# Performance work log

Hardware: AMD Instinct MI355X
Metric: run time of the kernel (lower is better)

Reference implementation:

```python
import jax, jax.numpy as jnp
import numpy as np

H = 16
W = 16
THRESH = 1.0
B = 32

# NOTE: [5.0, 1.0] reproduces the (likely buggy) constant in the original source.
SRC_POINTS = jnp.array([[0.0,0.0],[0.5,0.0],[1.0,0.0],[0.0,0.5],[0.5,0.5],[1.0,0.5],[0.0,1.0],[5.0,1.0],[1.0,1.0]], dtype=jnp.float32)

def _conv(x, w, stride, padding):
    return jax.lax.conv_general_dilated(x, w, (stride, stride), padding, dimension_numbers=('NHWC', 'HWIO', 'NHWC'))

def _tps_u(r):
    return r * r * jnp.log(r + 1e-6)

def _pdist(a, b):
    # a [...,2], b [n,2] -> [..., n] euclidean distances (eps for sqrt-at-0 safety)
    return jnp.sqrt(jnp.sum((a[..., None, :] - b) ** 2, axis=-1) + 1e-12)

def _tps_fit(ctrl, values):
    # cheind/py-thin-plate-spline TPS.fit with reduced=True. ctrl [n,2], values [n] -> theta [n+2]
    n = ctrl.shape[0]
    K = _tps_u(_pdist(ctrl, ctrl))
    P = jnp.concatenate([jnp.ones((n, 1), ctrl.dtype), ctrl], axis=1)
    A = jnp.zeros((n + 3, n + 3), ctrl.dtype)
    A = A.at[:n, :n].set(K).at[:n, n:].set(P).at[n:, :n].set(P.T)
    v = jnp.zeros(n + 3, ctrl.dtype).at[:n].set(values)
    theta = jnp.linalg.solve(A, v)
    return theta[1:]

def _tps_z(pts, ctrl, theta):
    # pts [m,2], theta reduced [n+2] -> [m]
    U = _tps_u(_pdist(pts, ctrl))
    w, a = theta[:-3], theta[-3:]
    w = jnp.concatenate([-jnp.sum(w, keepdims=True), w])
    return U @ w + a[0] + pts[:, 0] * a[1] + pts[:, 1] * a[2]

def _inlier_mask(geo):
    # geo [18] -> mask [H, W, H, W], mask[a_y, a_x, b_y, b_x]
    mv = geo.reshape(9, 2)
    dst = SRC_POINTS + mv
    delta = SRC_POINTS - dst  # c_src - c_dst (tps_theta_from_points)
    th_x = _tps_fit(dst, delta[:, 0])
    th_y = _tps_fit(dst, delta[:, 1])
    xs = jnp.linspace(0.0, 1.0, W)
    ys = jnp.linspace(0.0, 1.0, H)
    gx, gy = jnp.meshgrid(xs, ys)  # [H, W], gx varies along b_x
    pts = jnp.stack([gx.ravel(), gy.ravel()], axis=-1)
    ax = (gx + _tps_z(pts, dst, th_x).reshape(H, W)) * (H - 1)  # grid[...,0]*(map_size[0]-1)
    ay = (gy + _tps_z(pts, dst, th_y).reshape(H, W)) * (W - 1)
    # integer x in [ceil(ax-t), floor(ax+t)] clipped to [0,W-1]  <=>  |x - ax| <= t for x in range
    ix = jnp.arange(W, dtype=ax.dtype)
    iy = jnp.arange(H, dtype=ay.dtype)
    mx = jnp.abs(ix[:, None, None] - ax[None]) <= THRESH  # [W(a_x), H(b_y), W(b_x)]
    my = jnp.abs(iy[:, None, None] - ay[None]) <= THRESH  # [H(a_y), H(b_y), W(b_x)]
    return (my[:, None] & mx[None]).astype(jnp.float32)   # [H, W, H, W]

def _forward(image_A, image_B, W1, W2, W3, W4, Wr1, Wr2, Wd, bd):
    def feat(img):
        x = jax.nn.relu(_conv(img, W1, 2, 'SAME'))   # 256 -> 128
        x = jax.nn.relu(_conv(x, W2, 2, 'SAME'))     # 128 -> 64
        x = jax.nn.relu(_conv(x, W3, 2, 'SAME'))     # 64 -> 32
        x = jax.nn.relu(_conv(x, W4, 2, 'SAME'))     # 32 -> 16
        return x / (jnp.linalg.norm(x, axis=-1, keepdims=True) + 1e-6)  # channelwise l2 norm
    fA = feat(image_A)
    fB = feat(image_B)
    corr = jnp.einsum('bijc,bklc->bijkl', fA, fB)    # [B, H, W, H, W]
    b = corr.shape[0]
    r = corr.reshape(b, H, W, H * W)
    r = jax.nn.relu(_conv(r, Wr1, 1, 'VALID'))       # 16 -> 10
    r = jax.nn.relu(_conv(r, Wr2, 1, 'VALID'))       # 10 -> 6
    geo = r.reshape(b, -1) @ Wd + bd                 # [B, 18]
    # tf.numpy_function blocks gradients -> stop_gradient on the mask path
    masks = jax.lax.stop_gradient(jax.vmap(_inlier_mask)(geo))
    return jnp.sum(corr * masks, axis=(1, 2, 3, 4))  # [B]

def setup_inputs():
    key = jax.random.key(0)
    ks = jax.random.split(key, 10)
    s = 0.05
    return {
        'image_A': jax.random.normal(ks[0], (B, 256, 256, 3), jnp.float32),
        'image_B': jax.random.normal(ks[1], (B, 256, 256, 3), jnp.float32),
        'W1': jax.random.normal(ks[2], (3, 3, 3, 64), jnp.float32) * s,
        'W2': jax.random.normal(ks[3], (3, 3, 64, 128), jnp.float32) * s,
        'W3': jax.random.normal(ks[4], (3, 3, 128, 256), jnp.float32) * s,
        'W4': jax.random.normal(ks[5], (3, 3, 256, 512), jnp.float32) * s,
        'Wr1': jax.random.normal(ks[6], (7, 7, 256, 128), jnp.float32) * s,
        'Wr2': jax.random.normal(ks[7], (5, 5, 128, 64), jnp.float32) * s,
        'Wd': jax.random.normal(ks[8], (2304, 18), jnp.float32) * s,
        'bd': jnp.zeros((18,), jnp.float32),
    }

def reference(image_A, image_B, W1, W2, W3, W4, Wr1, Wr2, Wd, bd):
    return _forward(image_A, image_B, W1, W2, W3, W4, Wr1, Wr2, Wd, bd)
```

## Files before the change

kernel.cpp:

```cpp
#include <hip/hip_runtime.h>
#include <math.h>


typedef __attribute__((ext_vector_type(8))) _Float16 f16x8;
typedef __attribute__((ext_vector_type(4))) _Float16 f16x4;
typedef __attribute__((ext_vector_type(4))) float f32x4;

__device__ __forceinline__ unsigned short f2h(float f) {
  return __builtin_bit_cast(unsigned short, (_Float16)f);
}

__device__ __forceinline__ void gl16(const unsigned short* g, _Float16* l) {
  auto* gp = (const __attribute__((address_space(1))) unsigned int*)(g);
  auto* lp = (__attribute__((address_space(3))) unsigned int*)(l);
  __builtin_amdgcn_global_load_lds(gp, lp, 16, 0, 0);
}

__global__ __launch_bounds__(256) void prep_all(
    const float* __restrict__ W1, const float* __restrict__ W2,
    const float* __restrict__ W3, const float* __restrict__ W4,
    const float* __restrict__ Wr1, const float* __restrict__ Wr2,
    unsigned short* __restrict__ WT1, unsigned short* __restrict__ WT2,
    unsigned short* __restrict__ WT3, unsigned short* __restrict__ WT4,
    unsigned short* __restrict__ WTr1, unsigned short* __restrict__ WTr2,
    float* __restrict__ ZPf) {
  long idx = (long)blockIdx.x * 256 + threadIdx.x;
  if (idx < 1024) { ZPf[idx] = 0.f; return; }
  idx -= 1024;
  if (idx < 2048) {
    const int o = (int)idx >> 5, k = (int)idx & 31;
    WT1[idx] = (k < 27) ? f2h(W1[(size_t)k * 64 + o]) : (unsigned short)0;
    return;
  }
  idx -= 2048;
  if (idx < 73728) {
    const int k = (int)idx / 128, o = (int)idx % 128;
    WT2[(size_t)o * 576 + k] = f2h(W2[idx]);
    return;
  }
  idx -= 73728;
  if (idx < 294912) {
    const int k = (int)idx / 256, o = (int)idx % 256;
    WT3[(size_t)o * 1152 + k] = f2h(W3[idx]);
    return;
  }
  idx -= 294912;
  if (idx < 1179648) {
    const int k = (int)idx / 512, o = (int)idx % 512;
    WT4[(size_t)o * 2304 + k] = f2h(W4[idx]);
    return;
  }
  idx -= 1179648;
  if (idx < 1605632) {
    const int k = (int)idx / 128, o = (int)idx % 128;
    WTr1[(size_t)o * 12544 + k] = f2h(Wr1[idx]);
    return;
  }
  idx -= 1605632;
  if (idx < 204800) {
    const int k = (int)idx / 64, o = (int)idx % 64;
    WTr2[(size_t)o * 3200 + k] = f2h(Wr2[idx]);
  }
}

__global__ __launch_bounds__(256) void conv1_mfma(const float* __restrict__ inA,
                                                  const float* __restrict__ inB,
                                                  const unsigned short* __restrict__ wt1,
                                                  unsigned short* __restrict__ out) {
  const int i = blockIdx.x;
  const int b = blockIdx.y;
  const int tid = threadIdx.x;
  const int lane = tid & 63, wid = tid >> 6;
  const int lrow = lane & 15, quad = lane >> 4;

  __shared__ _Float16 Rows[3][776];
  __shared__ _Float16 OutB[8192];

  const float* __restrict__ img = (b < 32) ? inA : inB;
  const float* __restrict__ inb = img + (size_t)(b & 31) * 196608;
  const f16x4 z4 = {0, 0, 0, 0};
#pragma unroll
  for (int di = 0; di < 3; ++di) {
    const int y = 2 * i + di;
    if (tid < 192) {
      f16x4 h4 = z4;
      if (y < 256) {
        const float4 v4 = *(const float4*)(inb + (size_t)y * 768 + tid * 4);
        h4[0] = (_Float16)v4.x; h4[1] = (_Float16)v4.y;
        h4[2] = (_Float16)v4.z; h4[3] = (_Float16)v4.w;
      }
      *(f16x4*)&Rows[di][tid * 4] = h4;
    }
    if (tid < 3) Rows[di][768 + tid] = (_Float16)0.f;
  }
  __syncthreads();

  f16x8 bf[4];
#pragma unroll
  for (int ni = 0; ni < 4; ++ni)
    bf[ni] = *(const f16x8*)(wt1 + (ni * 16 + lrow) * 32 + quad * 8);

  f16x8 af[2];
#pragma unroll
  for (int mi = 0; mi < 2; ++mi) {
    const int j = wid * 32 + mi * 16 + lrow;
#pragma unroll
    for (int s = 0; s < 8; ++s) {
      const int k = quad * 8 + s;
      if (k < 27) {
        const int di = k / 9, dj = (k / 3) % 3, c = k % 3;
        af[mi][s] = Rows[di][(2 * j + dj) * 3 + c];
      } else {
        af[mi][s] = (_Float16)0.f;
      }
    }
  }

  f32x4 acc[2][4];
#pragma unroll
  for (int mi = 0; mi < 2; ++mi)
#pragma unroll
    for (int ni = 0; ni < 4; ++ni) {
      const f32x4 z = {0.f, 0.f, 0.f, 0.f};
      acc[mi][ni] = __builtin_amdgcn_mfma_f32_16x16x32_f16(af[mi], bf[ni], z, 0, 0, 0);
    }

#pragma unroll
  for (int mi = 0; mi < 2; ++mi)
#pragma unroll
    for (int ni = 0; ni < 4; ++ni)
#pragma unroll
      for (int r = 0; r < 4; ++r) {
        const int j = wid * 32 + mi * 16 + quad * 4 + r;
        const int ch = ni * 16 + lrow;
        OutB[j * 64 + (ch ^ (((j >> 2) & 3) << 4))] =
            (_Float16)fmaxf(acc[mi][ni][r], 0.f);
      }
  __syncthreads();

  unsigned short* __restrict__ ob = out + (((size_t)b * 128 + i) * 128) * 64;
#pragma unroll
  for (int q2 = 0; q2 < 4; ++q2) {
    const int v = tid + 256 * q2;
    const int j = v >> 3, c0 = (v & 7) * 8;
    const f16x8 pack = *(const f16x8*)&OutB[j * 64 + (c0 ^ (((j >> 2) & 3) << 4))];
    *(f16x8*)&ob[(size_t)j * 64 + c0] = pack;
  }
}

template <int BM, int BN, int CIN, int COUT, int KH, int KW, int STRIDE,
          int SAMEPAD, int SPLIT, int SK, int BATB, int OUTF32, int RELU>
__global__ __launch_bounds__(256) void tile_conv(
    const unsigned short* __restrict__ in, const unsigned short* __restrict__ wt,
    unsigned short* __restrict__ outh, float* __restrict__ outf,
    const unsigned short* __restrict__ zp,
    int Hin, int Win, int Hout, int Wout, int aLo, int bLo) {
  constexpr int CPT = CIN / 64;
  constexpr int LA = BM / 32;
  constexpr int LB = BN / 32;
  constexpr int KTOT = KH * KW * CIN;
  constexpr int MT = BM / 32;
  constexpr int NT = BN / 32;
  constexpr int PL = 1 + SPLIT;
  constexpr int LPS = PL * (LA + LB);
  constexpr unsigned WCN =
      (unsigned)((LPS & 0xF) | (0x7 << 4) | (0xF << 8) | ((LPS >> 4) << 14));
  constexpr unsigned WC0 = (unsigned)((0x7 << 4) | (0xF << 8));
  __shared__ _Float16 As[2][PL * BM * 64];
  __shared__ _Float16 Bs[2][PL * BN * 64];
  static_assert(SK > 1 || (size_t)BM * BN <= sizeof(As) / sizeof(_Float16),
                "bounce must fit in As");

  const int t = threadIdx.x;
  const int lane = t & 63, wid = t >> 6;
  const int lrow = lane & 15, quad = lane >> 4;
  const int m0 = blockIdx.x * BM;
  const int n0 = blockIdx.y * BN;

  const int q8 = ((t & 7) ^ ((t >> 3) & 7)) * 8;

  int pixB[LA], iS[LA], jS[LA];
#pragma unroll
  for (int i = 0; i < LA; ++i) {
    const int r = (t >> 3) + 32 * i;
    const int m = m0 + r;
    const int j = m % Wout;
    const int t2 = m / Wout;
    const int ii = t2 % Hout;
    const int b = t2 / Hout;
    iS[i] = ii * STRIDE;
    jS[i] = j * STRIDE;
    pixB[i] = ((b * Hin + iS[i]) * Win + jS[i]) * CIN + q8;
  }
  const unsigned short* wb = wt;
  if (BATB) wb += (size_t)(m0 / (Hout * Wout)) * COUT * KTOT;
  int bofB[LB];
#pragma unroll
  for (int i = 0; i < LB; ++i) {
    const int r = (t >> 3) + 32 * i;
    bofB[i] = (n0 + r) * KTOT + q8;
  }

  f32x4 acc[MT][NT];
#pragma unroll
  for (int mi = 0; mi < MT; ++mi)
#pragma unroll
    for (int ni = 0; ni < NT; ++ni) acc[mi][ni] = {0.f, 0.f, 0.f, 0.f};

  const int mB = (wid >> 1) * (BM / 2);
  const int nB = (wid & 1) * (BN / 2);

  int tap_lo = 0, tap_hi = KH * KW;
  if (SK > 1) {
    tap_lo = (int)blockIdx.z * KH * KW / SK;
    tap_hi = ((int)blockIdx.z + 1) * KH * KW / SK;
  }
  const int ch_lo = tap_lo * CPT, ch_hi = tap_hi * CPT;

  auto stage = [&](int buf, int ch) {
    const int tap = ch / CPT;
    const int c0 = (ch % CPT) * 64;
    const int di = tap / KW, dj = tap % KW;
    const int toff = (di * Win + dj) * CIN + c0;
    const int woff = tap * CIN + c0;
#pragma unroll
    for (int i = 0; i < LA; ++i) {
      const bool ok = !SAMEPAD || ((iS[i] + di < Hin) && (jS[i] + dj < Win));
      const unsigned short* s0 = ok ? in + pixB[i] + toff : zp + q8;
      gl16(s0, &As[buf][t * 8 + 2048 * i]);
      if (SPLIT) {
        const unsigned short* s1 = ok ? in + pixB[i] + toff + aLo : zp + q8;
        gl16(s1, &As[buf][BM * 64 + t * 8 + 2048 * i]);
      }
    }
#pragma unroll
    for (int i = 0; i < LB; ++i) {
      gl16(wb + bofB[i] + woff, &Bs[buf][t * 8 + 2048 * i]);
      if (SPLIT)
        gl16(wb + bofB[i] + woff + bLo, &Bs[buf][BN * 64 + t * 8 + 2048 * i]);
    }
  };

  stage(0, ch_lo);
  if (ch_lo + 1 < ch_hi) stage(1, ch_lo + 1);
  int cur = 0;
  for (int ch = ch_lo; ch < ch_hi; ++ch) {
    if (ch + 1 < ch_hi) __builtin_amdgcn_s_waitcnt(WCN);
    else __builtin_amdgcn_s_waitcnt(WC0);
    __builtin_amdgcn_sched_barrier(0);
    __builtin_amdgcn_s_barrier();
    __builtin_amdgcn_sched_barrier(0);
#pragma unroll
    for (int ks = 0; ks < 2; ++ks) {
      f16x8 af[MT], bf[NT], al[MT], bl[NT];
#pragma unroll
      for (int mi = 0; mi < MT; ++mi) {
        const int row = mB + mi * 16 + lrow;
        const int off = row * 64 + (((ks * 4 + quad) ^ (row & 7)) * 8);
        af[mi] = *(const f16x8*)&As[cur][off];
        if (SPLIT) al[mi] = *(const f16x8*)&As[cur][BM * 64 + off];
      }
#pragma unroll
      for (int ni = 0; ni < NT; ++ni) {
        const int row = nB + ni * 16 + lrow;
        const int off = row * 64 + (((ks * 4 + quad) ^ (row & 7)) * 8);
        bf[ni] = *(const f16x8*)&Bs[cur][off];
        if (SPLIT) bl[ni] = *(const f16x8*)&Bs[cur][BN * 64 + off];
      }
#pragma unroll
      for (int mi = 0; mi < MT; ++mi)
#pragma unroll
        for (int ni = 0; ni < NT; ++ni) {
          if (SPLIT) {
            acc[mi][ni] = __builtin_amdgcn_mfma_f32_16x16x32_f16(af[mi], bl[ni],
                                                                 acc[mi][ni], 0, 0, 0);
            acc[mi][ni] = __builtin_amdgcn_mfma_f32_16x16x32_f16(al[mi], bf[ni],
                                                                 acc[mi][ni], 0, 0, 0);
          }
          acc[mi][ni] = __builtin_amdgcn_mfma_f32_16x16x32_f16(af[mi], bf[ni],
                                                               acc[mi][ni], 0, 0, 0);
        }
    }
    __builtin_amdgcn_sched_barrier(0);
    __builtin_amdgcn_s_barrier();
    __builtin_amdgcn_sched_barrier(0);
    if (ch + 2 < ch_hi) stage(cur, ch + 2);
    cur ^= 1;
  }

  if (SK > 1) {
    const size_t slice = (size_t)blockIdx.z * ((size_t)gridDim.x * BM * COUT);
#pragma unroll
    for (int mi = 0; mi < MT; ++mi)
#pragma unroll
      for (int ni = 0; ni < NT; ++ni)
#pragma unroll
        for (int r = 0; r < 4; ++r) {
          const int row = m0 + mB + mi * 16 + quad * 4 + r;
          const int col = n0 + nB + ni * 16 + lrow;
          outf[slice + (size_t)row * COUT + col] = acc[mi][ni][r];
        }
  } else {
    _Float16* bounce = &As[0][0];
#pragma unroll
    for (int mi = 0; mi < MT; ++mi)
#pragma unroll
      for (int ni = 0; ni < NT; ++ni)
#pragma unroll
        for (int r = 0; r < 4; ++r) {
          const int row = mB + mi * 16 + quad * 4 + r;
          const int col = nB + ni * 16 + lrow;
          float v = acc[mi][ni][r];
          if (OUTF32) {
            outf[(size_t)(m0 + row) * COUT + n0 + col] = v;
          } else if (RELU) {
            v = fmaxf(v, 0.f);
          }
          bounce[row * BN + (col ^ (((row >> 2) & 3) << 4))] = (_Float16)v;
        }
    __syncthreads();
    constexpr int VPT = (BM * BN / 8) / 256;
#pragma unroll
    for (int q2 = 0; q2 < VPT; ++q2) {
      const int v = t + 256 * q2;
      const int rowL = v / (BN / 8);
      const int c0 = (v % (BN / 8)) * 8;
      const f16x8 pack =
          *(const f16x8*)&bounce[rowL * BN + (c0 ^ (((rowL >> 2) & 3) << 4))];
      *(f16x8*)&outh[(size_t)(m0 + rowL) * COUT + n0 + c0] = pack;
    }
  }
}

template <int MT, int NT, int CIN, int COUT, int KH, int KW, int SK>
__global__ __launch_bounds__(256) void gemm_conv(
    const unsigned short* __restrict__ in, const unsigned short* __restrict__ wt,
    float* __restrict__ outf, int Hin, int Win, int Hout, int Wout) {
  const int KTOT = KH * KW * CIN;
  const int lane = threadIdx.x & 63;
  const int wid = threadIdx.x >> 6;
  const int lrow = lane & 15;
  const int quad = lane >> 4;
  const int m0 = (blockIdx.x * 4 + wid) * (16 * MT);
  const int n0 = blockIdx.y * (16 * NT);

  int pix[MT];
#pragma unroll
  for (int mi = 0; mi < MT; ++mi) {
    const int m = m0 + mi * 16 + lrow;
    const int j = m % Wout;
    const int t = m / Wout;
    const int i = t % Hout;
    const int b = t / Hout;
    pix[mi] = (b * Hin + i) * Win + j;
  }
  const unsigned short* brow[NT];
#pragma unroll
  for (int ni = 0; ni < NT; ++ni)
    brow[ni] = wt + (size_t)(n0 + ni * 16 + lrow) * KTOT + quad * 8;

  f32x4 acc[MT][NT];
#pragma unroll
  for (int mi = 0; mi < MT; ++mi)
#pragma unroll
    for (int ni = 0; ni < NT; ++ni) acc[mi][ni] = {0.f, 0.f, 0.f, 0.f};

  const int tap_lo = (int)blockIdx.z * KH * KW / SK;
  const int tap_hi = ((int)blockIdx.z + 1) * KH * KW / SK;
  for (int tap = tap_lo; tap < tap_hi; ++tap) {
    const int di = tap / KW, dj = tap % KW;
    const unsigned short* ap[MT];
#pragma unroll
    for (int mi = 0; mi < MT; ++mi)
      ap[mi] = in + ((size_t)pix[mi] + di * Win + dj) * CIN + quad * 8;
    const int ko = tap * CIN;
#pragma unroll
    for (int c0 = 0; c0 < CIN; c0 += 32) {
      f16x8 ah[MT], bh[NT];
#pragma unroll
      for (int mi = 0; mi < MT; ++mi) ah[mi] = *(const f16x8*)(ap[mi] + c0);
#pragma unroll
      for (int ni = 0; ni < NT; ++ni) bh[ni] = *(const f16x8*)(brow[ni] + ko + c0);
#pragma unroll
      for (int mi = 0; mi < MT; ++mi)
#pragma unroll
        for (int ni = 0; ni < NT; ++ni)
          acc[mi][ni] = __builtin_amdgcn_mfma_f32_16x16x32_f16(ah[mi], bh[ni],
                                                               acc[mi][ni], 0, 0, 0);
    }
  }
  const size_t slice = (size_t)blockIdx.z * ((size_t)gridDim.x * 64 * MT * COUT);
#pragma unroll
  for (int mi = 0; mi < MT; ++mi)
#pragma unroll
    for (int ni = 0; ni < NT; ++ni)
#pragma unroll
      for (int r = 0; r < 4; ++r) {
        const int row = m0 + mi * 16 + quad * 4 + r;
        const int col = n0 + ni * 16 + lrow;
        outf[slice + (size_t)row * COUT + col] = acc[mi][ni][r];
      }
}

__global__ __launch_bounds__(256) void sum_relu_s(const float* __restrict__ p,
                                                  unsigned short* __restrict__ o,
                                                  int n, int parts) {
  const int idx = blockIdx.x * 256 + threadIdx.x;
  if (idx < n) {
    float v = 0.f;
    for (int s = 0; s < parts; ++s) v += p[(size_t)s * n + idx];
    o[idx] = f2h(fmaxf(v, 0.f));
  }
}
__global__ __launch_bounds__(256) void sum_relu_f(const float* __restrict__ p,
                                                  float* __restrict__ o,
                                                  int n, int parts) {
  const int idx = blockIdx.x * 256 + threadIdx.x;
  if (idx < n) {
    float v = 0.f;
    for (int s = 0; s < parts; ++s) v += p[(size_t)s * n + idx];
    o[idx] = fmaxf(v, 0.f);
  }
}

__global__ __launch_bounds__(64) void l2norm_k(const unsigned short* __restrict__ x,
                                               unsigned short* __restrict__ y,
                                               int loOff) {
  const int lane = threadIdx.x;
  const f16x8 v = *(const f16x8*)(x + (size_t)blockIdx.x * 512 + lane * 8);
  float f[8];
  float s = 0.f;
#pragma unroll
  for (int k = 0; k < 8; ++k) {
    f[k] = (float)v[k];
    s += f[k] * f[k];
  }
#pragma unroll
  for (int off = 32; off; off >>= 1) s += __shfl_xor(s, off, 64);
  const float inv = 1.f / (sqrtf(s) + 1e-6f);
  f16x8 vh, vl;
#pragma unroll
  for (int k = 0; k < 8; ++k) {
    const float nv = f[k] * inv;
    const _Float16 hi = (_Float16)nv;
    vh[k] = hi;
    vl[k] = (_Float16)(nv - (float)hi);
  }
  unsigned short* ph = y + (size_t)blockIdx.x * 512 + lane * 8;
  *(f16x8*)ph = vh;
  *(f16x8*)(ph + (size_t)loOff) = vl;
}

__global__ __launch_bounds__(64) void dense_k(const float* __restrict__ r2,
                                              const float* __restrict__ wd,
                                              const float* __restrict__ bd,
                                              float* __restrict__ geo) {
  const int o = blockIdx.x;
  const int b = blockIdx.y;
  const int lane = threadIdx.x;
  const float* __restrict__ rb = r2 + (size_t)b * 2304;
  float s = 0.f;
  for (int k = lane; k < 2304; k += 64) s += rb[k] * wd[(size_t)k * 18 + o];
#pragma unroll
  for (int off = 32; off; off >>= 1) s += __shfl_xor(s, off, 64);
  if (lane == 0) geo[b * 18 + o] = s + bd[o];
}

__device__ __forceinline__ float tps_u(float r) { return r * r * logf(r + 1e-6f); }

__global__ __launch_bounds__(64) void tps_k(const float* __restrict__ geo,
                                            float* __restrict__ axb,
                                            float* __restrict__ ayb) {
  const int b = blockIdx.x;
  const int tid = threadIdx.x;
  __shared__ float M[12][14];
  __shared__ float fel[12];
  __shared__ float dxs[9], dys[9];
  __shared__ float th[2][12];
  __shared__ float sW[2][9];
  __shared__ float sA[2][3];
  __shared__ int sPiv;

  const float srcx[9] = {0.f, 0.5f, 1.f, 0.f, 0.5f, 1.f, 0.f, 5.f, 1.f};
  const float srcy[9] = {0.f, 0.f, 0.f, 0.5f, 0.5f, 0.5f, 1.f, 1.f, 1.f};

  if (tid < 9) {
    const float mx = geo[b * 18 + 2 * tid], my = geo[b * 18 + 2 * tid + 1];
    dxs[tid] = srcx[tid] + mx;
    dys[tid] = srcy[tid] + my;
    M[tid][12] = -mx;
    M[tid][13] = -my;
  } else if (tid < 12) {
    M[tid][12] = 0.f;
    M[tid][13] = 0.f;
  }
  __syncthreads();
  for (int e = tid; e < 81; e += 64) {
    const int p = e / 9, q = e % 9;
    const float ddx = dxs[p] - dxs[q], ddy = dys[p] - dys[q];
    const float r = sqrtf(ddx * ddx + ddy * ddy + 1e-12f);
    M[p][q] = tps_u(r);
  }
  if (tid < 9) {
    M[tid][9] = 1.f;  M[tid][10] = dxs[tid]; M[tid][11] = dys[tid];
    M[9][tid] = 1.f;  M[10][tid] = dxs[tid]; M[11][tid] = dys[tid];
  } else if (tid < 12) {
    M[tid][9] = 0.f; M[tid][10] = 0.f; M[tid][11] = 0.f;
  }
  __syncthreads();

  for (int k = 0; k < 12; ++k) {
    if (tid == 0) {
      int piv = k;
      float best = fabsf(M[k][k]);
      for (int r = k + 1; r < 12; ++r) {
        const float v = fabsf(M[r][k]);
        if (v > best) { best = v; piv = r; }
      }
      sPiv = piv;
    }
    __syncthreads();
    const int piv = sPiv;
    if (piv != k && tid < 14) {
      const float tmp = M[k][tid];
      M[k][tid] = M[piv][tid];
      M[piv][tid] = tmp;
    }
    __syncthreads();
    if (tid > k && tid < 12) fel[tid] = M[tid][k] / M[k][k];
    __syncthreads();
    for (int e = tid; e < (11 - k) * 14; e += 64) {
      const int r = k + 1 + e / 14, cc = e % 14;
      if (cc >= k) M[r][cc] -= fel[r] * M[k][cc];
    }
    __syncthreads();
  }

  const int grp = tid >> 4;
  const int cc = tid & 15;
  for (int k = 11; k >= 0; --k) {
    float prod = 0.f;
    if (grp < 2 && cc > k && cc < 12) prod = M[k][cc] * th[grp][cc];
#pragma unroll
    for (int off = 8; off; off >>= 1) prod += __shfl_xor(prod, off, 16);
    if (grp < 2 && cc == 0) th[grp][k] = (M[k][12 + grp] - prod) / M[k][k];
    __syncthreads();
  }

  if (tid < 2) {
    float sw = 0.f;
    for (int p = 1; p < 9; ++p) {
      sW[tid][p] = th[tid][p];
      sw += th[tid][p];
    }
    sW[tid][0] = -sw;
    sA[tid][0] = th[tid][9];
    sA[tid][1] = th[tid][10];
    sA[tid][2] = th[tid][11];
  }
  __syncthreads();

  for (int p = tid; p < 256; p += 64) {
    const int pi = p >> 4, pj = p & 15;
    const float x = pj * (1.f / 15.f), y = pi * (1.f / 15.f);
    float zx = sA[0][0] + x * sA[0][1] + y * sA[0][2];
    float zy = sA[1][0] + x * sA[1][1] + y * sA[1][2];
#pragma unroll
    for (int c = 0; c < 9; ++c) {
      const float ddx = x - dxs[c], ddy = y - dys[c];
      const float r = sqrtf(ddx * ddx + ddy * ddy + 1e-12f);
      const float u = tps_u(r);
      zx += u * sW[0][c];
      zy += u * sW[1][c];
    }
    axb[b * 256 + p] = (x + zx) * 15.f;
    ayb[b * 256 + p] = (y + zy) * 15.f;
  }
}

__global__ __launch_bounds__(256) void masksum_k(const float* __restrict__ corr,
                                                 const float* __restrict__ axb,
                                                 const float* __restrict__ ayb,
                                                 float* __restrict__ out) {
  const int b = blockIdx.x;
  const int pB = threadIdx.x;
  const float ax = axb[b * 256 + pB];
  const float ay = ayb[b * 256 + pB];
  const float* __restrict__ cb = corr + (size_t)b * 65536;
  float s = 0.f;
  for (int i = 0; i < 16; ++i) {
    if (fabsf((float)i - ay) <= 1.0f) {
      const float* __restrict__ ci = cb + (size_t)i * 16 * 256 + pB;
      for (int j = 0; j < 16; ++j) {
        if (fabsf((float)j - ax) <= 1.0f) s += ci[(size_t)j * 256];
      }
    }
  }
  __shared__ float sm[256];
  sm[pB] = s;
  __syncthreads();
  for (int off = 128; off; off >>= 1) {
    if (pB < off) sm[pB] += sm[pB + off];
    __syncthreads();
  }
  if (pB == 0) out[b] = sm[0];
}

extern "C" void kernel_launch(void* const* d_in, const int* in_sizes, int n_in,
                              void* d_out, int out_size, void* d_ws, size_t ws_size,
                              hipStream_t stream) {
  const float* imgA = (const float*)d_in[0];
  const float* imgB = (const float*)d_in[1];
  const float* W1 = (const float*)d_in[2];
  const float* W2 = (const float*)d_in[3];
  const float* W3 = (const float*)d_in[4];
  const float* W4 = (const float*)d_in[5];
  const float* Wr1 = (const float*)d_in[6];
  const float* Wr2 = (const float*)d_in[7];
  const float* Wd = (const float*)d_in[8];
  const float* bd = (const float*)d_in[9];

  float* ws = (float*)d_ws;
  unsigned short* WT2 = (unsigned short*)(ws + 0);
  unsigned short* WT3 = (unsigned short*)(ws + 36864);
  unsigned short* WT4 = (unsigned short*)(ws + 184320);
  unsigned short* WTr1 = (unsigned short*)(ws + 774144);
  unsigned short* WTr2 = (unsigned short*)(ws + 1576960);
  unsigned short* FEATs = (unsigned short*)(ws + 1679360);
  unsigned short* S3both = (unsigned short*)(ws + 5873664);
  unsigned short* S2both = (unsigned short*)(ws + 14262272);
  unsigned short* S1both = (unsigned short*)(ws + 31039488);
  unsigned short* FEATsp = (unsigned short*)(ws + 5873664);
  float* CORRf = ws + 14262272;
  unsigned short* CORRh = (unsigned short*)(ws + 16359424);
  float* R1p = ws + 17408000;
  unsigned short* R1h = (unsigned short*)(ws + 27648000);
  float* R2p = ws + 27750400;
  float* R2f = ws + 29593600;
  float* GEOb = ws + 29667328;
  float* AXb = ws + 29667904;
  float* AYb = ws + 29676096;
  unsigned short* WT1 = (unsigned short*)(ws + 64593920);
  float* ZPf = ws + 64594944;
  const unsigned short* ZP = (const unsigned short*)ZPf;

  prep_all<<<13132, 256, 0, stream>>>(W1, W2, W3, W4, Wr1, Wr2,
                                      WT1, WT2, WT3, WT4, WTr1, WTr2, ZPf);

  conv1_mfma<<<dim3(128, 64), 256, 0, stream>>>(imgA, imgB, WT1, S1both);
  tile_conv<128, 128, 64, 128, 3, 3, 2, 1, 0, 1, 0, 0, 1>
      <<<dim3(2048, 1), 256, 0, stream>>>(S1both, WT2, S2both, nullptr, ZP,
                                          128, 128, 64, 64, 0, 0);
  tile_conv<128, 128, 128, 256, 3, 3, 2, 1, 0, 1, 0, 0, 1>
      <<<dim3(512, 2), 256, 0, stream>>>(S2both, WT3, S3both, nullptr, ZP,
                                         64, 64, 32, 32, 0, 0);
  tile_conv<128, 128, 256, 512, 3, 3, 2, 1, 0, 1, 0, 0, 1>
      <<<dim3(128, 4), 256, 0, stream>>>(S3both, WT4, FEATs, nullptr, ZP,
                                         32, 32, 16, 16, 0, 0);

  l2norm_k<<<16384, 64, 0, stream>>>(FEATs, FEATsp, 8388608);
  tile_conv<64, 64, 512, 256, 1, 1, 1, 0, 1, 1, 1, 1, 0>
      <<<dim3(128, 4), 256, 0, stream>>>(FEATsp, FEATsp + 4194304, CORRh, CORRf,
                                         ZP, 16, 16, 16, 16, 8388608, 8388608);
  tile_conv<128, 128, 256, 128, 7, 7, 1, 0, 0, 25, 0, 0, 0>
      <<<dim3(25, 1, 25), 256, 0, stream>>>(CORRh, WTr1, nullptr, R1p, ZP,
                                            16, 16, 10, 10, 0, 0);
  sum_relu_s<<<1600, 256, 0, stream>>>(R1p, R1h, 409600, 25);
  gemm_conv<1, 4, 128, 64, 5, 5, 25>
      <<<dim3(18, 1, 25), 256, 0, stream>>>(R1h, WTr2, R2p, 10, 10, 6, 6);
  sum_relu_f<<<288, 256, 0, stream>>>(R2p, R2f, 73728, 25);
  dense_k<<<dim3(18, 32), 64, 0, stream>>>(R2f, Wd, bd, GEOb);
  tps_k<<<32, 64, 0, stream>>>(GEOb, AXb, AYb);
  masksum_k<<<32, 256, 0, stream>>>(CORRf, AXb, AYb, (float*)d_out);
}
```

Before: 434.4 us.

## Use triple-buffered 32-wide K chunks with a single barrier per step

The shared-memory pipeline of the implicit-GEMM conv kernel changes from two 64-channel buffers to three 32-channel buffers carved from one LDS array. The prefetch for chunk ch+2 now goes out right after the top barrier, before the MFMA work, so the trailing barrier per iteration can be dropped. The swizzle is adjusted to the 32-wide rows, and fragment offsets are hoisted out of the loop. The aim is better load/compute overlap and a smaller LDS footprint. In exchange there are twice as many loop iterations and smaller loads per step, and an extra sync is added before the epilogue reuses the buffer.

```diff
diff --git a/kernel.cpp b/kernel.cpp
--- a/kernel.cpp
+++ b/kernel.cpp
@@ -155,21 +155,22 @@
     unsigned short* __restrict__ outh, float* __restrict__ outf,
     const unsigned short* __restrict__ zp,
     int Hin, int Win, int Hout, int Wout, int aLo, int bLo) {
-  constexpr int CPT = CIN / 64;
-  constexpr int LA = BM / 32;
-  constexpr int LB = BN / 32;
+  constexpr int CPT = CIN / 32;
+  constexpr int LA = BM / 64;
+  constexpr int LB = BN / 64;
   constexpr int KTOT = KH * KW * CIN;
   constexpr int MT = BM / 32;
   constexpr int NT = BN / 32;
   constexpr int PL = 1 + SPLIT;
   constexpr int LPS = PL * (LA + LB);
+  constexpr int ASTR = PL * BM * 32;
+  constexpr int BSTR = PL * BN * 32;
   constexpr unsigned WCN =
       (unsigned)((LPS & 0xF) | (0x7 << 4) | (0xF << 8) | ((LPS >> 4) << 14));
   constexpr unsigned WC0 = (unsigned)((0x7 << 4) | (0xF << 8));
-  __shared__ _Float16 As[2][PL * BM * 64];
-  __shared__ _Float16 Bs[2][PL * BN * 64];
-  static_assert(SK > 1 || (size_t)BM * BN <= sizeof(As) / sizeof(_Float16),
-                "bounce must fit in As");
+  __shared__ _Float16 SH[3 * (ASTR + BSTR)];
+  static_assert(SK > 1 || (size_t)BM * BN <= (size_t)3 * (ASTR + BSTR),
+                "bounce must fit in SH");
 
   const int t = threadIdx.x;
   const int lane = t & 63, wid = t >> 6;
@@ -177,12 +178,12 @@
   const int m0 = blockIdx.x * BM;
   const int n0 = blockIdx.y * BN;
 
-  const int q8 = ((t & 7) ^ ((t >> 3) & 7)) * 8;
+  const int q8 = ((t & 3) ^ ((t >> 3) & 3)) * 8;
 
   int pixB[LA], iS[LA], jS[LA];
 #pragma unroll
   for (int i = 0; i < LA; ++i) {
-    const int r = (t >> 3) + 32 * i;
+    const int r = (t >> 2) + 64 * i;
     const int m = m0 + r;
     const int j = m % Wout;
     const int t2 = m / Wout;
@@ -197,7 +198,7 @@
   int bofB[LB];
 #pragma unroll
   for (int i = 0; i < LB; ++i) {
-    const int r = (t >> 3) + 32 * i;
+    const int r = (t >> 2) + 64 * i;
     bofB[i] = (n0 + r) * KTOT + q8;
   }
 
@@ -209,6 +210,18 @@
 
   const int mB = (wid >> 1) * (BM / 2);
   const int nB = (wid & 1) * (BN / 2);
+
+  int offA[MT], offB[NT];
+#pragma unroll
+  for (int mi = 0; mi < MT; ++mi) {
+    const int row = mB + mi * 16 + lrow;
+    offA[mi] = row * 32 + ((quad ^ ((row >> 1) & 3)) * 8);
+  }
+#pragma unroll
+  for (int ni = 0; ni < NT; ++ni) {
+    const int row = nB + ni * 16 + lrow;
+    offB[ni] = row * 32 + ((quad ^ ((row >> 1) & 3)) * 8);
+  }
 
   int tap_lo = 0, tap_hi = KH * KW;
   if (SK > 1) {
@@ -219,25 +232,27 @@
 
   auto stage = [&](int buf, int ch) {
     const int tap = ch / CPT;
-    const int c0 = (ch % CPT) * 64;
+    const int c0 = (ch & (CPT - 1)) * 32;
     const int di = tap / KW, dj = tap % KW;
     const int toff = (di * Win + dj) * CIN + c0;
     const int woff = tap * CIN + c0;
+    _Float16* aB = SH + buf * ASTR;
+    _Float16* bB = SH + 3 * ASTR + buf * BSTR;
 #pragma unroll
     for (int i = 0; i < LA; ++i) {
       const bool ok = !SAMEPAD || ((iS[i] + di < Hin) && (jS[i] + dj < Win));
       const unsigned short* s0 = ok ? in + pixB[i] + toff : zp + q8;
-      gl16(s0, &As[buf][t * 8 + 2048 * i]);
+      gl16(s0, aB + t * 8 + 2048 * i);
       if (SPLIT) {
         const unsigned short* s1 = ok ? in + pixB[i] + toff + aLo : zp + q8;
-        gl16(s1, &As[buf][BM * 64 + t * 8 + 2048 * i]);
+        gl16(s1, aB + BM * 32 + t * 8 + 2048 * i);
       }
     }
 #pragma unroll
     for (int i = 0; i < LB; ++i) {
-      gl16(wb + bofB[i] + woff, &Bs[buf][t * 8 + 2048 * i]);
+      gl16(wb + bofB[i] + woff, bB + t * 8 + 2048 * i);
       if (SPLIT)
-        gl16(wb + bofB[i] + woff + bLo, &Bs[buf][BN * 64 + t * 8 + 2048 * i]);
+        gl16(wb + bofB[i] + woff + bLo, bB + BN * 32 + t * 8 + 2048 * i);
     }
   };
 
@@ -250,22 +265,20 @@
     __builtin_amdgcn_sched_barrier(0);
     __builtin_amdgcn_s_barrier();
     __builtin_amdgcn_sched_barrier(0);
-#pragma unroll
-    for (int ks = 0; ks < 2; ++ks) {
+    if (ch + 2 < ch_hi) stage(cur == 0 ? 2 : cur - 1, ch + 2);
+    {
+      const _Float16* aB = SH + cur * ASTR;
+      const _Float16* bB = SH + 3 * ASTR + cur * BSTR;
       f16x8 af[MT], bf[NT], al[MT], bl[NT];
 #pragma unroll
       for (int mi = 0; mi < MT; ++mi) {
-        const int row = mB + mi * 16 + lrow;
-        const int off = row * 64 + (((ks * 4 + quad) ^ (row & 7)) * 8);
-        af[mi] = *(const f16x8*)&As[cur][off];
-        if (SPLIT) al[mi] = *(const f16x8*)&As[cur][BM * 64 + off];
+        af[mi] = *(const f16x8*)&aB[offA[mi]];
+        if (SPLIT) al[mi] = *(const f16x8*)&aB[BM * 32 + offA[mi]];
       }
 #pragma unroll
       for (int ni = 0; ni < NT; ++ni) {
-        const int row = nB + ni * 16 + lrow;
-        const int off = row * 64 + (((ks * 4 + quad) ^ (row & 7)) * 8);
-        bf[ni] = *(const f16x8*)&Bs[cur][off];
-        if (SPLIT) bl[ni] = *(const f16x8*)&Bs[cur][BN * 64 + off];
+        bf[ni] = *(const f16x8*)&bB[offB[ni]];
+        if (SPLIT) bl[ni] = *(const f16x8*)&bB[BN * 32 + offB[ni]];
       }
 #pragma unroll
       for (int mi = 0; mi < MT; ++mi)
@@ -281,11 +294,7 @@
                                                                acc[mi][ni], 0, 0, 0);
         }
     }
-    __builtin_amdgcn_sched_barrier(0);
-    __builtin_amdgcn_s_barrier();
-    __builtin_amdgcn_sched_barrier(0);
-    if (ch + 2 < ch_hi) stage(cur, ch + 2);
-    cur ^= 1;
+    cur = (cur == 2) ? 0 : cur + 1;
   }
 
   if (SK > 1) {
@@ -301,7 +310,8 @@
           outf[slice + (size_t)row * COUT + col] = acc[mi][ni][r];
         }
   } else {
-    _Float16* bounce = &As[0][0];
+    __syncthreads();
+    _Float16* bounce = &SH[0];
 #pragma unroll
     for (int mi = 0; mi < MT; ++mi)
 #pragma unroll
```

Result: faster. 417.5 us (-3.9%).
